# Kernel optimization log

Measured on AMD Instinct MI355X. Metric: run time of the kernel, lower is better.

## Reference

```python
import jax, jax.numpy as jnp
import numpy as np

SQRT2 = np.float32(np.sqrt(2.0))


def _depthwise(x, h, axis):
    """Symmetric-pad depthwise 1D conv along `axis` (2=col/height, 3=row/width).
    Emulates dtcwt_slim ColFilter/RowFilter: prep_filt flips the taps, then
    F.conv2d cross-correlates with groups=C (same taps for every channel).
    x: (B,C,H,W), h: (L,) with L odd -> same-size output."""
    C = x.shape[1]
    L = h.shape[0]
    m = L // 2
    hf = jnp.flip(h)  # prep_filt stores h[::-1]
    if axis == 2:
        xp = jnp.pad(x, ((0, 0), (0, 0), (m, m), (0, 0)), mode='symmetric')
        ker = jnp.tile(hf[None, None, :, None], (C, 1, 1, 1))  # (C,1,L,1)
    else:
        xp = jnp.pad(x, ((0, 0), (0, 0), (0, 0), (m, m)), mode='symmetric')
        ker = jnp.tile(hf[None, None, None, :], (C, 1, 1, 1))  # (C,1,1,L)
    return jax.lax.conv_general_dilated(
        xp, ker, window_strides=(1, 1), padding='VALID',
        dimension_numbers=('NCHW', 'OIHW', 'NCHW'), feature_group_count=C)


def colfilter(x, h):
    return _depthwise(x, h, axis=2)


def rowfilter(x, h):
    return _depthwise(x, h, axis=3)


def c2q(w_r, w_i):
    """Complex pair of subbands -> real quad-interleaved image.
    w_r, w_i: (B,C,2,H,W) -> (B,C,2H,2W)."""
    w1r, w1i = w_r[:, :, 0], w_i[:, :, 0]
    w2r, w2i = w_r[:, :, 1], w_i[:, :, 1]
    x1 = w1r + w2r          # y[::2,  ::2]
    x2 = w1i + w2i          # y[::2, 1::2]
    x3 = w1i - w2i          # y[1::2, ::2]
    x4 = w2r - w1r          # y[1::2,1::2]
    B, C, H, W = x1.shape
    top = jnp.stack([x1, x2], axis=-1).reshape(B, C, H, 2 * W)
    bot = jnp.stack([x3, x4], axis=-1).reshape(B, C, H, 2 * W)
    y = jnp.stack([top, bot], axis=-2).reshape(B, C, 2 * H, 2 * W)
    return y / SQRT2


def setup_inputs() -> dict:
    key = jax.random.key(0)
    k1, k2, k3, k4, k5, k6 = jax.random.split(key, 6)
    B, C, H, W = 8, 64, 256, 256
    Yl = jax.random.normal(k1, (B, C, H, W), dtype=jnp.float32)
    Yhr = jax.random.normal(k2, (B, C, 6, H // 2, W // 2), dtype=jnp.float32)
    Yhi = jax.random.normal(k3, (B, C, 6, H // 2, W // 2), dtype=jnp.float32)
    # near_sym_b_bp synthesis filters (fixed, non-trainable buffers): 13/19/13 taps
    g0o = jax.random.normal(k4, (13,), dtype=jnp.float32) * 0.3
    g1o = jax.random.normal(k5, (19,), dtype=jnp.float32) * 0.3
    g2o = jax.random.normal(k6, (13,), dtype=jnp.float32) * 0.3
    return {"Yl": Yl, "Yhr": Yhr, "Yhi": Yhi, "g0o": g0o, "g1o": g1o, "g2o": g2o}


def reference(Yl, Yhr, Yhi, g0o, g1o, g2o):
    # orientation pairs: (15,165)->lh uses bands 0,5; (75,105)->hl bands 2,3;
    # (45,135 bandpass)->hh bands 1,4
    lh = c2q(Yhr[:, :, 0:6:5], Yhi[:, :, 0:6:5])
    hl = c2q(Yhr[:, :, 2:4:1], Yhi[:, :, 2:4:1])
    hh = c2q(Yhr[:, :, 1:5:3], Yhi[:, :, 1:5:3])
    y1 = colfilter(Yl, g0o) + colfilter(lh, g1o)
    y2 = colfilter(hl, g0o)
    y2bp = colfilter(hh, g2o)
    y = rowfilter(y1, g0o) + rowfilter(y2, g1o) + rowfilter(y2bp, g2o)
    return y
```

## Files before the change

### kernel.cpp

```cpp
#include <hip/hip_runtime.h>

#define PW 90
#define IS2 0.70710678118654752f

__device__ __forceinline__ int symidx(int t, int n) {
    t = (t < 0) ? (-1 - t) : t;
    return (t >= n) ? (2 * n - 1 - t) : t;
}

#define SB() __builtin_amdgcn_sched_barrier(0)

__device__ __forceinline__ void col13_yl(
    float (&acc)[32], const float* __restrict__ ylp,
    const float* __restrict__ taps, int r0, int cc)
{
    #pragma unroll
    for (int pi = 0; pi < 44; ++pi) {
        int rr = symidx(r0 - 6 + pi, 256);
        float v = ylp[rr * 256 + cc];
        #pragma unroll
        for (int j = 0; j < 13; ++j) {
            int ro = pi + j - 12;
            if (ro >= 0 && ro < 32) acc[ro] = fmaf(taps[j], v, acc[ro]);
        }
    }
}

__device__ __forceinline__ void col13_c2q(
    float (&acc)[32], const float* __restrict__ yhr, const float* __restrict__ yhi,
    int bA, int bB, const float* __restrict__ taps, int r0, int cc)
{
    const int cp = cc & 1;
    const int j2 = cc >> 1;
    #pragma unroll
    for (int pi = 0; pi < 44; ++pi) {
        int rr = symidx(r0 - 6 + pi, 256);
        int rp = rr & 1;
        int i2 = rr >> 1;
        const float* base = (((rp ^ cp) != 0) ? yhi : yhr) + (i2 * 128 + j2);
        float A  = base[bA * 16384];
        float Bv = base[bB * 16384];
        float vA = (rp & cp)       ? -A  : A;
        float vB = (rp & (cp ^ 1)) ? -Bv : Bv;
        float v = (vA + vB) * IS2;
        #pragma unroll
        for (int j = 0; j < 13; ++j) {
            int ro = pi + j - 12;
            if (ro >= 0 && ro < 32) acc[ro] = fmaf(taps[j], v, acc[ro]);
        }
    }
}

__device__ __forceinline__ void col19_c2q(
    float (&acc)[32], const float* __restrict__ yhr, const float* __restrict__ yhi,
    const float* __restrict__ taps, int r0, int cc)
{
    const int bA = 0, bB = 5;
    const int cp = cc & 1;
    const int j2 = cc >> 1;
    #pragma unroll
    for (int pi = 0; pi < 50; ++pi) {
        int rr = symidx(r0 - 9 + pi, 256);
        int rp = rr & 1;
        int i2 = rr >> 1;
        const float* base = (((rp ^ cp) != 0) ? yhi : yhr) + (i2 * 128 + j2);
        float A  = base[0 * 16384];
        float Bv = base[5 * 16384];
        float vA = (rp & cp)       ? -A  : A;
        float vB = (rp & (cp ^ 1)) ? -Bv : Bv;
        float v = (vA + vB) * IS2;
        #pragma unroll
        for (int j = 0; j < 19; ++j) {
            int ro = pi + j - 18;
            if (ro >= 0 && ro < 32) acc[ro] = fmaf(taps[j], v, acc[ro]);
        }
    }
}

template<int NU>
__device__ __forceinline__ void load_pairs(float* buf,
    const float* __restrict__ pEA, const float* __restrict__ pEB,
    const float* __restrict__ pOA, const float* __restrict__ pOB,
    int vof)
{
    #pragma unroll
    for (int u = 0; u < NU; ++u) {
        buf[4*u+0] = pEA[vof + u * 128];
        buf[4*u+1] = pEB[vof + u * 128];
        buf[4*u+2] = pOA[vof + u * 128];
        buf[4*u+3] = pOB[vof + u * 128];
    }
}

template<int L, int EPI0, int UB, int NU>
__device__ __forceinline__ void consume_pairs(float (&acc)[32], const float* buf,
                                              float sgn, const float* __restrict__ taps)
{
    #pragma unroll
    for (int u = 0; u < NU; ++u) {
        float ve = (buf[4*u+0] + buf[4*u+1]) * IS2;
        float vo = (buf[4*u+2] - buf[4*u+3]) * sgn;
        const int pi = EPI0 + 2 * (UB + u);
        #pragma unroll
        for (int j = 0; j < L; ++j) {
            int ro = pi + j - (L - 1);
            if (ro >= 0 && ro < 32) acc[ro] = fmaf(taps[j], ve, acc[ro]);
        }
        #pragma unroll
        for (int j = 0; j < L; ++j) {
            int ro = pi + 1 + j - (L - 1);
            if (ro >= 0 && ro < 32) acc[ro] = fmaf(taps[j], vo, acc[ro]);
        }
    }
}

template<int L, int EPI0, int NPT, int C>
__device__ __forceinline__ void c2q_pipe3(
    float (&acc)[32],
    const float* __restrict__ pEA, const float* __restrict__ pEB,
    const float* __restrict__ pOA, const float* __restrict__ pOB,
    int vof, float sgn, const float* __restrict__ taps)
{
    constexpr int N0 = NPT - 4 * C;
    static_assert(N0 > 0 && N0 <= 8, "chunking");
    constexpr int A0 = 0, B0 = N0, C0 = N0 + C, A1 = N0 + 2 * C, B1 = N0 + 3 * C;
    float bufA[4 * ((N0 > C) ? N0 : C)], bufB[4 * C], bufC[4 * C];
    load_pairs<N0>(bufA, pEA, pEB, pOA, pOB, vof + A0 * 128);
    SB();
    load_pairs<C>(bufB, pEA, pEB, pOA, pOB, vof + B0 * 128);
    SB();
    load_pairs<C>(bufC, pEA, pEB, pOA, pOB, vof + C0 * 128);
    SB();
    consume_pairs<L, EPI0, A0, N0>(acc, bufA, sgn, taps);
    SB();
    load_pairs<C>(bufA, pEA, pEB, pOA, pOB, vof + A1 * 128);
    SB();
    consume_pairs<L, EPI0, B0, C>(acc, bufB, sgn, taps);
    SB();
    load_pairs<C>(bufB, pEA, pEB, pOA, pOB, vof + B1 * 128);
    SB();
    consume_pairs<L, EPI0, C0, C>(acc, bufC, sgn, taps);
    SB();
    consume_pairs<L, EPI0, A1, C>(acc, bufA, sgn, taps);
    SB();
    consume_pairs<L, EPI0, B1, C>(acc, bufB, sgn, taps);
}

template<int NT>
__device__ __forceinline__ void load_rows(float* buf, const float* __restrict__ p, int t0)
{
    #pragma unroll
    for (int t = 0; t < NT; ++t) buf[t] = p[(t0 + t) * 256];
}

template<int TB, int NT>
__device__ __forceinline__ void consume_rows(float (&acc)[32], const float* buf,
                                             const float* __restrict__ taps)
{
    #pragma unroll
    for (int t = 0; t < NT; ++t) {
        float v = buf[t];
        const int pi = TB + t;
        #pragma unroll
        for (int j = 0; j < 13; ++j) {
            int ro = pi + j - 12;
            if (ro >= 0 && ro < 32) acc[ro] = fmaf(taps[j], v, acc[ro]);
        }
    }
}

__device__ __forceinline__ void yl_pipe3(float (&acc)[32], const float* __restrict__ p,
                                         const float* __restrict__ g0)
{
    float bufA[10], bufB[10], bufC[10];
    load_rows<4>(bufA, p, 0);
    SB();
    load_rows<10>(bufB, p, 4);
    SB();
    load_rows<10>(bufC, p, 14);
    SB();
    consume_rows<0, 4>(acc, bufA, g0);
    SB();
    load_rows<10>(bufA, p, 24);
    SB();
    consume_rows<4, 10>(acc, bufB, g0);
    SB();
    load_rows<10>(bufB, p, 34);
    SB();
    consume_rows<14, 10>(acc, bufC, g0);
    SB();
    consume_rows<24, 10>(acc, bufA, g0);
    SB();
    consume_rows<34, 10>(acc, bufB, g0);
}

extern "C" __global__ __launch_bounds__(512, 4) void dtcwt_inv(
    const float* __restrict__ Yl, const float* __restrict__ Yhr,
    const float* __restrict__ Yhi,
    const float* __restrict__ g0, const float* __restrict__ g1,
    const float* __restrict__ g2, float* __restrict__ out)
{
    __shared__ __align__(16) float sU[3][32][PW];

    const int tid = threadIdx.x;
    const int wg  = blockIdx.x;
    const int swz = (wg & 7) * 2048 + (wg >> 3);
    const int plane = swz >> 5;
    const int bt = swz & 31;
    const int bx = bt & 3;
    const int by = bt >> 2;
    const int r0 = by * 32;
    const int c0 = bx * 64;

    const float* ylp = Yl  + (size_t)plane * 65536;
    const float* yhr = Yhr + (size_t)plane * 6 * 16384;
    const float* yhi = Yhi + (size_t)plane * 6 * 16384;

    const bool rowInterior = (by >= 1) && (by <= 6);

    const int role = tid >> 7;
    const int lr   = tid & 127;

    float acc[32];
    #pragma unroll
    for (int i = 0; i < 32; ++i) acc[i] = 0.0f;
    int ti = -1;

    if (rowInterior) {
        if (role == 0) {
            if (lr < 76) {
                ti = lr + 6;
                int cc = symidx(c0 + lr - 6, 256);
                yl_pipe3(acc, ylp + (r0 - 6) * 256 + cc, g0);
            }
        } else if (role == 1) {
            if (lr < 76) {
                ti = lr + 6;
                int cc = symidx(c0 + lr - 6, 256);
                int cp = cc & 1, j2 = cc >> 1;
                const float* pE = cp ? yhi : yhr;
                const float* pO = cp ? yhr : yhi;
                float sgn = cp ? -IS2 : IS2;
                int vof = ((r0 - 10) >> 1) * 128 + j2;
                c2q_pipe3<19, -1, 26, 5>(acc,
                    pE + 0 * 16384, pE + 5 * 16384,
                    pO + 0 * 16384, pO + 5 * 16384, vof, sgn, g1);
            }
        } else if (role == 2) {
            if (lr < 82) {
                ti = lr + 3;
                int cc = symidx(c0 + lr - 9, 256);
                int cp = cc & 1, j2 = cc >> 1;
                const float* pE = cp ? yhi : yhr;
                const float* pO = cp ? yhr : yhi;
                float sgn = cp ? -IS2 : IS2;
                int vof = ((r0 - 6) >> 1) * 128 + j2;
                c2q_pipe3<13, 0, 22, 5>(acc,
                    pE + 2 * 16384, pE + 3 * 16384,
                    pO + 2 * 16384, pO + 3 * 16384, vof, sgn, g0);
            }
        } else {
            if (lr < 76) {
                ti = lr + 6;
                int cc = symidx(c0 + lr - 6, 256);
                int cp = cc & 1, j2 = cc >> 1;
                const float* pE = cp ? yhi : yhr;
                const float* pO = cp ? yhr : yhi;
                float sgn = cp ? -IS2 : IS2;
                int vof = ((r0 - 6) >> 1) * 128 + j2;
                c2q_pipe3<13, 0, 22, 5>(acc,
                    pE + 1 * 16384, pE + 4 * 16384,
                    pO + 1 * 16384, pO + 4 * 16384, vof, sgn, g2);
            }
        }
    } else {
        if (role == 0) {
            if (lr < 76) {
                ti = lr + 6;
                int cc = symidx(c0 + ti - 12, 256);
                col13_yl(acc, ylp, g0, r0, cc);
            }
        } else if (role == 1) {
            if (lr < 76) {
                ti = lr + 6;
                int cc = symidx(c0 + ti - 12, 256);
                col19_c2q(acc, yhr, yhi, g1, r0, cc);
            }
        } else if (role == 2) {
            if (lr < 82) {
                ti = lr + 3;
                int cc = symidx(c0 + ti - 12, 256);
                col13_c2q(acc, yhr, yhi, 2, 3, g0, r0, cc);
            }
        } else {
            if (lr < 76) {
                ti = lr + 6;
                int cc = symidx(c0 + ti - 12, 256);
                col13_c2q(acc, yhr, yhi, 1, 4, g2, r0, cc);
            }
        }
    }

    if (ti >= 0 && role != 1) {
        const int bi = (role == 0) ? 0 : (role == 2 ? 1 : 2);
        #pragma unroll
        for (int ro = 0; ro < 32; ++ro) sU[bi][ro][ti] = acc[ro];
    }
    __syncthreads();

    if (role == 1 && ti >= 0) {
        #pragma unroll
        for (int ro = 0; ro < 32; ++ro) sU[0][ro][ti] += acc[ro];
    }

    const int cg = tid & 15;
    const int r2 = tid >> 4;
    const int cb = 4 * cg;

    float w2v[28];
    #pragma unroll
    for (int k = 0; k < 14; ++k) {
        float2 a = *(const float2*)&sU[1][r2][cb + 2 * k];
        w2v[2*k] = a.x; w2v[2*k+1] = a.y;
    }
    float w3v[20];
    #pragma unroll
    for (int k = 0; k < 10; ++k) {
        float2 a = *(const float2*)&sU[2][r2][cb + 4 + 2 * k];
        w3v[2*k] = a.x; w3v[2*k+1] = a.y;
    }
    __syncthreads();

    float w1v[20];
    #pragma unroll
    for (int k = 0; k < 10; ++k) {
        float2 a = *(const float2*)&sU[0][r2][cb + 4 + 2 * k];
        w1v[2*k] = a.x; w1v[2*k+1] = a.y;
    }

    float4 res;
    float* op = (float*)&res;
    #pragma unroll
    for (int q = 0; q < 4; ++q) {
        float s = 0.0f;
        #pragma unroll
        for (int j = 0; j < 13; ++j) s = fmaf(g0[j], w1v[q + 14 - j], s);
        #pragma unroll
        for (int j = 0; j < 19; ++j) s = fmaf(g1[j], w2v[q + 21 - j], s);
        #pragma unroll
        for (int j = 0; j < 13; ++j) s = fmaf(g2[j], w3v[q + 14 - j], s);
        op[q] = s;
    }
    *(float4*)&out[(size_t)plane * 65536 + (size_t)(r0 + r2) * 256 + (c0 + cb)] = res;
}

extern "C" void kernel_launch(void* const* d_in, const int* in_sizes, int n_in,
                              void* d_out, int out_size, void* d_ws, size_t ws_size,
                              hipStream_t stream) {
    const float* Yl  = (const float*)d_in[0];
    const float* Yhr = (const float*)d_in[1];
    const float* Yhi = (const float*)d_in[2];
    const float* g0  = (const float*)d_in[3];
    const float* g1  = (const float*)d_in[4];
    const float* g2  = (const float*)d_in[5];
    float* out = (float*)d_out;

    dim3 grid(16384, 1, 1);
    dim3 block(512, 1, 1);
    dtcwt_inv<<<grid, block, 0, stream>>>(Yl, Yhr, Yhi, g0, g1, g2, out);
}
```

Before: 317.6 us.

## Widen tile to 128 columns with 1024-thread blocks to cut halo overhead

Each workgroup now covers a 32x128 output tile instead of 32x64, using 1024 threads with 256 per role. The column-filter stage now computes 140–146 halo-extended columns per role instead of 76–82, so redundant halo work and reloads per output drop. The three intermediate shared buffers are split and the row-filter indexing is re-based. Larger blocks raise per-block LDS use and register pressure under launch_bounds(1024,4), which may reduce occupancy.

```diff
diff --git a/kernel.cpp b/kernel.cpp
--- a/kernel.cpp
+++ b/kernel.cpp
@@ -1,6 +1,5 @@
 #include <hip/hip_runtime.h>
 
-#define PW 90
 #define IS2 0.70710678118654752f
 
 __device__ __forceinline__ int symidx(int t, int n) {
@@ -55,7 +54,6 @@
     float (&acc)[32], const float* __restrict__ yhr, const float* __restrict__ yhi,
     const float* __restrict__ taps, int r0, int cc)
 {
-    const int bA = 0, bB = 5;
     const int cp = cc & 1;
     const int j2 = cc >> 1;
     #pragma unroll
@@ -194,23 +192,25 @@
     consume_rows<34, 10>(acc, bufB, g0);
 }
 
-extern "C" __global__ __launch_bounds__(512, 4) void dtcwt_inv(
+extern "C" __global__ __launch_bounds__(1024, 4) void dtcwt_inv(
     const float* __restrict__ Yl, const float* __restrict__ Yhr,
     const float* __restrict__ Yhi,
     const float* __restrict__ g0, const float* __restrict__ g1,
     const float* __restrict__ g2, float* __restrict__ out)
 {
-    __shared__ __align__(16) float sU[3][32][PW];
+    __shared__ __align__(16) float sU1[32][142];
+    __shared__ __align__(16) float sU2[32][146];
+    __shared__ __align__(16) float sU3[32][142];
 
     const int tid = threadIdx.x;
     const int wg  = blockIdx.x;
-    const int swz = (wg & 7) * 2048 + (wg >> 3);
-    const int plane = swz >> 5;
-    const int bt = swz & 31;
-    const int bx = bt & 3;
-    const int by = bt >> 2;
+    const int swz = (wg & 7) * 1024 + (wg >> 3);
+    const int plane = swz >> 4;
+    const int bt = swz & 15;
+    const int bx = bt & 1;
+    const int by = bt >> 1;
     const int r0 = by * 32;
-    const int c0 = bx * 64;
+    const int c0 = bx * 128;
 
     const float* ylp = Yl  + (size_t)plane * 65536;
     const float* yhr = Yhr + (size_t)plane * 6 * 16384;
@@ -218,8 +218,8 @@
 
     const bool rowInterior = (by >= 1) && (by <= 6);
 
-    const int role = tid >> 7;
-    const int lr   = tid & 127;
+    const int role = tid >> 8;
+    const int lr   = tid & 255;
 
     float acc[32];
     #pragma unroll
@@ -228,15 +228,15 @@
 
     if (rowInterior) {
         if (role == 0) {
-            if (lr < 76) {
-                ti = lr + 6;
-                int cc = symidx(c0 + lr - 6, 256);
+            if (lr < 140) {
+                ti = lr;
+                int cc = symidx(c0 - 6 + lr, 256);
                 yl_pipe3(acc, ylp + (r0 - 6) * 256 + cc, g0);
             }
         } else if (role == 1) {
-            if (lr < 76) {
-                ti = lr + 6;
-                int cc = symidx(c0 + lr - 6, 256);
+            if (lr < 140) {
+                ti = lr;
+                int cc = symidx(c0 - 6 + lr, 256);
                 int cp = cc & 1, j2 = cc >> 1;
                 const float* pE = cp ? yhi : yhr;
                 const float* pO = cp ? yhr : yhi;
@@ -247,9 +247,9 @@
                     pO + 0 * 16384, pO + 5 * 16384, vof, sgn, g1);
             }
         } else if (role == 2) {
-            if (lr < 82) {
-                ti = lr + 3;
-                int cc = symidx(c0 + lr - 9, 256);
+            if (lr < 146) {
+                ti = lr;
+                int cc = symidx(c0 - 9 + lr, 256);
                 int cp = cc & 1, j2 = cc >> 1;
                 const float* pE = cp ? yhi : yhr;
                 const float* pO = cp ? yhr : yhi;
@@ -260,9 +260,9 @@
                     pO + 2 * 16384, pO + 3 * 16384, vof, sgn, g0);
             }
         } else {
-            if (lr < 76) {
-                ti = lr + 6;
-                int cc = symidx(c0 + lr - 6, 256);
+            if (lr < 140) {
+                ti = lr;
+                int cc = symidx(c0 - 6 + lr, 256);
                 int cp = cc & 1, j2 = cc >> 1;
                 const float* pE = cp ? yhi : yhr;
                 const float* pO = cp ? yhr : yhi;
@@ -275,66 +275,73 @@
         }
     } else {
         if (role == 0) {
-            if (lr < 76) {
-                ti = lr + 6;
-                int cc = symidx(c0 + ti - 12, 256);
+            if (lr < 140) {
+                ti = lr;
+                int cc = symidx(c0 - 6 + lr, 256);
                 col13_yl(acc, ylp, g0, r0, cc);
             }
         } else if (role == 1) {
-            if (lr < 76) {
-                ti = lr + 6;
-                int cc = symidx(c0 + ti - 12, 256);
+            if (lr < 140) {
+                ti = lr;
+                int cc = symidx(c0 - 6 + lr, 256);
                 col19_c2q(acc, yhr, yhi, g1, r0, cc);
             }
         } else if (role == 2) {
-            if (lr < 82) {
-                ti = lr + 3;
-                int cc = symidx(c0 + ti - 12, 256);
+            if (lr < 146) {
+                ti = lr;
+                int cc = symidx(c0 - 9 + lr, 256);
                 col13_c2q(acc, yhr, yhi, 2, 3, g0, r0, cc);
             }
         } else {
-            if (lr < 76) {
-                ti = lr + 6;
-                int cc = symidx(c0 + ti - 12, 256);
+            if (lr < 140) {
+                ti = lr;
+                int cc = symidx(c0 - 6 + lr, 256);
                 col13_c2q(acc, yhr, yhi, 1, 4, g2, r0, cc);
             }
         }
     }
 
-    if (ti >= 0 && role != 1) {
-        const int bi = (role == 0) ? 0 : (role == 2 ? 1 : 2);
-        #pragma unroll
-        for (int ro = 0; ro < 32; ++ro) sU[bi][ro][ti] = acc[ro];
+    if (ti >= 0) {
+        if (role == 0) {
+            #pragma unroll
+            for (int ro = 0; ro < 32; ++ro) sU1[ro][ti] = acc[ro];
+        } else if (role == 2) {
+            #pragma unroll
+            for (int ro = 0; ro < 32; ++ro) sU2[ro][ti] = acc[ro];
+        } else if (role == 3) {
+            #pragma unroll
+            for (int ro = 0; ro < 32; ++ro) sU3[ro][ti] = acc[ro];
+        }
     }
     __syncthreads();
 
     if (role == 1 && ti >= 0) {
         #pragma unroll
-        for (int ro = 0; ro < 32; ++ro) sU[0][ro][ti] += acc[ro];
-    }
-
-    const int cg = tid & 15;
-    const int r2 = tid >> 4;
+        for (int ro = 0; ro < 32; ++ro) sU1[ro][ti] += acc[ro];
+    }
+
+    const int cg = tid & 31;
+    const int r2 = tid >> 5;
     const int cb = 4 * cg;
 
-    float w2v[28];
-    #pragma unroll
-    for (int k = 0; k < 14; ++k) {
-        float2 a = *(const float2*)&sU[1][r2][cb + 2 * k];
+    float w2v[22];
+    #pragma unroll
+    for (int k = 0; k < 11; ++k) {
+        float2 a = *(const float2*)&sU2[r2][cb + 2 * k];
         w2v[2*k] = a.x; w2v[2*k+1] = a.y;
     }
-    float w3v[20];
-    #pragma unroll
-    for (int k = 0; k < 10; ++k) {
-        float2 a = *(const float2*)&sU[2][r2][cb + 4 + 2 * k];
+    float w3v[16];
+    #pragma unroll
+    for (int k = 0; k < 8; ++k) {
+        float2 a = *(const float2*)&sU3[r2][cb + 2 * k];
         w3v[2*k] = a.x; w3v[2*k+1] = a.y;
     }
     __syncthreads();
 
-    float w1v[20];
-    #pragma unroll
-    for (int k = 0; k < 10; ++k) {
-        float2 a = *(const float2*)&sU[0][r2][cb + 4 + 2 * k];
+    float w1v[16];
+    #pragma unroll
+    for (int k = 0; k < 8; ++k) {
+        float2 a = *(const float2*)&sU1[r2][cb + 2 * k];
         w1v[2*k] = a.x; w1v[2*k+1] = a.y;
     }
 
@@ -344,11 +351,11 @@
     for (int q = 0; q < 4; ++q) {
         float s = 0.0f;
         #pragma unroll
-        for (int j = 0; j < 13; ++j) s = fmaf(g0[j], w1v[q + 14 - j], s);
-        #pragma unroll
-        for (int j = 0; j < 19; ++j) s = fmaf(g1[j], w2v[q + 21 - j], s);
-        #pragma unroll
-        for (int j = 0; j < 13; ++j) s = fmaf(g2[j], w3v[q + 14 - j], s);
+        for (int j = 0; j < 13; ++j) s = fmaf(g0[j], w1v[q + 12 - j], s);
+        #pragma unroll
+        for (int j = 0; j < 19; ++j) s = fmaf(g1[j], w2v[q + 18 - j], s);
+        #pragma unroll
+        for (int j = 0; j < 13; ++j) s = fmaf(g2[j], w3v[q + 12 - j], s);
         op[q] = s;
     }
     *(float4*)&out[(size_t)plane * 65536 + (size_t)(r0 + r2) * 256 + (c0 + cb)] = res;
@@ -365,7 +372,7 @@
     const float* g2  = (const float*)d_in[5];
     float* out = (float*)d_out;
 
-    dim3 grid(16384, 1, 1);
-    dim3 block(512, 1, 1);
+    dim3 grid(8192, 1, 1);
+    dim3 block(1024, 1, 1);
     dtcwt_inv<<<grid, block, 0, stream>>>(Yl, Yhr, Yhi, g0, g1, g2, out);
 }
```

After: 436.8 us. 1.38x slower.
